# Kernel tuning notes

Hardware: AMD Instinct MI355X
Metric: run time of the kernel (lower is better)

## Reference

```python
import jax, jax.numpy as jnp
import numpy as np

NUM_BEAM, NUM_NULL, NUM_BIN, NUM_CH = 8, 4, 257, 8
NUM_BLOCK, NUM_FRAME = 8, 500
ALPHA, LOW_FREQ, HIGH_FREQ = 0.35, 5, 70


def setup_inputs() -> dict:
    key = jax.random.key(0)
    k1, k2, k3, k4 = jax.random.split(key, 4)
    return {
        "input": jax.random.normal(k1, (NUM_BLOCK, NUM_FRAME, 2, NUM_BIN, NUM_CH), jnp.float32),
        "beam_id": jax.random.randint(k2, (NUM_BLOCK,), 0, NUM_BEAM),
        "targ_w": jax.random.normal(k3, (NUM_BEAM, 2, NUM_BIN, NUM_CH), jnp.float32),
        "null_w": jax.random.normal(k4, (NUM_BEAM, NUM_NULL, 2, NUM_BIN, NUM_CH), jnp.float32),
    }


def _forward(input, beam_id, targ_w, null_w):
    a = ALPHA
    xr, xi = input[:, :, 0], input[:, :, 1]            # (B,T,F,C)
    # target beamformer: select per-block complex weights (B,2,F,C)
    tw = targ_w[beam_id]
    twr, twi = tw[:, 0], tw[:, 1]                      # (B,F,C)
    tr = jnp.einsum('btfc,bfc->btf', xr, twr) - jnp.einsum('btfc,bfc->btf', xi, twi)
    ti = jnp.einsum('btfc,bfc->btf', xr, twi) + jnp.einsum('btfc,bfc->btf', xi, twr)
    tr, ti = tr[..., None], ti[..., None]              # (B,T,F,1)
    # null beamformer: (B,N,2,F,C)
    nw = null_w[beam_id]
    nwr, nwi = nw[:, :, 0], nw[:, :, 1]                # (B,N,F,C)
    nr = jnp.einsum('btfc,bnfc->btfn', xr, nwr) - jnp.einsum('btfc,bnfc->btfn', xi, nwi)
    ni = jnp.einsum('btfc,bnfc->btfn', xr, nwi) + jnp.einsum('btfc,bnfc->btfn', xi, nwr)
    # elementwise cross-spectra products (B,T,F,N)
    pr = tr * nr + ti * ni
    pi = ti * nr - tr * ni
    pw = jnp.mean(xr ** 2 + xi ** 2, axis=-1, keepdims=True)  # (B,T,F,1)

    # t = 0 (note: (1-alpha) scales only the FIRST product, as in the source)
    phi_r0 = (1.0 - a) * tr[:, 0] * nr[:, 0] + ti[:, 0] * ni[:, 0]
    phi_i0 = (1.0 - a) * ti[:, 0] * nr[:, 0] - tr[:, 0] * ni[:, 0]
    psd0 = (1.0 - a) * pw[:, 0]
    phi0 = jnp.sqrt(phi_r0 ** 2 + phi_i0 ** 2)
    dcf0 = jnp.clip(phi0 / (psd0 + 1e-13), 0.01, 1.0)

    def step(carry, xs):
        phi_r, phi_i, psd = carry
        pr_t, pi_t, pw_t = xs
        phi_r = a * phi_r + (1.0 - a) * pr_t
        phi_i = a * phi_i + (1.0 - a) * pi_t
        psd = a * psd + (1.0 - a) * pw_t
        phi = jnp.sqrt(phi_r ** 2 + phi_i ** 2)
        dcf_t = jnp.clip(phi / (psd + 1e-13), 0.01, 1.0)
        pre = jnp.sum(psd[:, LOW_FREQ:HIGH_FREQ, :], axis=1, keepdims=True)
        aft = jnp.sum(phi[:, LOW_FREQ:HIGH_FREQ, :], axis=1, keepdims=True)
        ratio = jnp.clip(aft / (pre + 1e-10), 0.01, 1.0)
        dcf_t = jnp.sqrt(dcf_t * ratio)
        return (phi_r, phi_i, psd), dcf_t

    xs = (jnp.moveaxis(pr[:, 1:], 1, 0),
          jnp.moveaxis(pi[:, 1:], 1, 0),
          jnp.moveaxis(pw[:, 1:], 1, 0))
    _, dcf_rest = jax.lax.scan(step, (phi_r0, phi_i0, psd0), xs)  # (T-1,B,F,N)
    dcf = jnp.concatenate([dcf0[None], dcf_rest], axis=0)
    dcf = jnp.moveaxis(dcf, 0, 1)                                 # (B,T,F,N)
    targ_out = jnp.stack([tr[..., 0], ti[..., 0]], axis=2)        # (B,T,2,F)
    return dcf, targ_out


def reference(input, beam_id, targ_w, null_w):
    return _forward(input, beam_id, targ_w, null_w)
```

## Files before the change

### kernel.cpp

```cpp
#include <hip/hip_runtime.h>

#define NB 8
#define NT 500
#define NF 257
#define NC 8
#define NNUL 4
#define LOWF 5
#define HIGHF 70
#define S_CHUNK 8
#define WARM 4
#define N_CHUNK 63
#define AL 0.35f

__device__ __forceinline__ float dot8(const float4& a0, const float4& a1,
                                      const float4& b0, const float4& b1) {
    return a0.x*b0.x + a0.y*b0.y + a0.z*b0.z + a0.w*b0.w
         + a1.x*b1.x + a1.y*b1.y + a1.z*b1.z + a1.w*b1.w;
}

__global__ __launch_bounds__(1024, 4) void dcf_fused_kernel(
    const float* __restrict__ x,
    const int* __restrict__ beam_id,
    const float* __restrict__ targ_w,
    const float* __restrict__ null_w,
    float* __restrict__ out)
{
    const int tid = threadIdx.x;
    const int bid = blockIdx.x;
    const int b  = bid & 7;
    const int k  = bid >> 3;
    const int t0 = k * S_CHUNK;
    const int te = min(NT, t0 + S_CHUNK);
    int ts = t0 - WARM; if (ts < 0) ts = 0;

    const int f = tid >> 2;
    const int n = tid & 3;
    const int wid = tid >> 6;
    const int lane = tid & 63;
    const bool extra = (tid < 4);

    __shared__ float s_w256[16 + 4 * 16];
    __shared__ float s_part[S_CHUNK][25];
    __shared__ float s_dcf[S_CHUNK][1028];

    const int beam = beam_id[b];
    const int pA = n & 1;
    const int offA = pA * (NF * NC);
    const int offB = (1 - pA) * (NF * NC);
    const int psel = (n == 1 || n == 2) ? 1 : 0;
    const float nsign = pA ? -1.f : 1.f;

    float4 tw0, tw1, nwA0, nwA1, nwB0, nwB1;
    {
        const float* tp = targ_w + ((size_t)(beam * 2 + psel) * NF + f) * NC;
        tw0 = *(const float4*)(tp);  tw1 = *(const float4*)(tp + 4);
        const float* qp = null_w + ((size_t)((beam * NNUL + n) * 2) * NF + f) * NC;
        nwA0 = *(const float4*)(qp + offA);  nwA1 = *(const float4*)(qp + offA + 4);
        nwB0 = *(const float4*)(qp + offB);  nwB1 = *(const float4*)(qp + offB + 4);
    }
    if (tid < 16) {
        int p = tid >> 3, c = tid & 7;
        s_w256[tid] = targ_w[((size_t)(beam * 2 + p) * NF + 256) * NC + c];
    } else if (tid < 80) {
        int i = tid - 16;
        int nn = i >> 4, p = (i >> 3) & 1, c = i & 7;
        s_w256[tid] = null_w[((size_t)((beam * NNUL + nn) * 2 + p) * NF + 256) * NC + c];
    }
    __syncthreads();

    float phi_r = 0.f, phi_i = 0.f, psd = 0.f;
    float phi_r2 = 0.f, phi_i2 = 0.f, psd2 = 0.f;
    const float a = AL, oma = 1.0f - AL;
    const size_t rowlen = 2 * NF * NC;
    const bool in_red = (f >= LOWF) && (f < HIGHF);

    const float* xrow = x + (size_t)(b * NT + ts) * rowlen + f * NC;
    float4 pA0 = *(const float4*)(xrow + offA);
    float4 pA1 = *(const float4*)(xrow + offA + 4);
    float4 pB0 = *(const float4*)(xrow + offB);
    float4 pB1 = *(const float4*)(xrow + offB + 4);

    float* outT = out + (size_t)NB * NT * NF * NNUL;

    for (int t = ts; t < te; ++t) {
        const float4 A0 = pA0, A1 = pA1, B0 = pB0, B1 = pB1;
        if (t + 1 < te) {
            const float* xr2 = x + (size_t)(b * NT + t + 1) * rowlen + f * NC;
            pA0 = *(const float4*)(xr2 + offA);
            pA1 = *(const float4*)(xr2 + offA + 4);
            pB0 = *(const float4*)(xr2 + offB);
            pB1 = *(const float4*)(xr2 + offB + 4);
        }

        const float d = dot8(A0, A1, tw0, tw1);
        const float e = __shfl_xor(d, 1);
        const float u = (n < 2) ? ((n == 0) ? (d - e) : (e - d)) : (d + e);
        const float v = __shfl_xor(u, 2);
        const float tr = (n < 2) ? u : v;
        const float ti = (n < 2) ? v : u;

        const float P = dot8(A0, A1, nwA0, nwA1);
        const float Q = dot8(B0, B1, nwB0, nwB1);
        const float nr = nsign * (P - Q);
        const float ni = dot8(A0, A1, nwB0, nwB1) + dot8(B0, B1, nwA0, nwA1);
        const float pw = (dot8(A0, A1, A0, A1) + dot8(B0, B1, B0, B1)) * 0.125f;

        if (t == 0) {
            phi_r = oma * tr * nr + ti * ni;
            phi_i = oma * ti * nr - tr * ni;
            psd   = oma * pw;
        } else {
            phi_r = a * phi_r + oma * (tr * nr + ti * ni);
            phi_i = a * phi_i + oma * (ti * nr - tr * ni);
            psd   = a * psd + oma * pw;
        }

        float tr2 = 0.f, ti2 = 0.f;
        if (extra) {
            const float* xw = x + (size_t)(b * NT + t) * rowlen + 256 * NC;
            const float4 eA0 = *(const float4*)(xw + offA);
            const float4 eA1 = *(const float4*)(xw + offA + 4);
            const float4 eB0 = *(const float4*)(xw + offB);
            const float4 eB1 = *(const float4*)(xw + offB + 4);
            const float4 etw0 = *(const float4*)&s_w256[psel * 8];
            const float4 etw1 = *(const float4*)&s_w256[psel * 8 + 4];
            const float* nq = &s_w256[16 + n * 16];
            const float4 enA0 = *(const float4*)(nq + pA * 8);
            const float4 enA1 = *(const float4*)(nq + pA * 8 + 4);
            const float4 enB0 = *(const float4*)(nq + (1 - pA) * 8);
            const float4 enB1 = *(const float4*)(nq + (1 - pA) * 8 + 4);
            const float d2 = dot8(eA0, eA1, etw0, etw1);
            const float e2 = __shfl_xor(d2, 1);
            const float u2 = (n < 2) ? ((n == 0) ? (d2 - e2) : (e2 - d2)) : (d2 + e2);
            const float v2 = __shfl_xor(u2, 2);
            tr2 = (n < 2) ? u2 : v2;
            ti2 = (n < 2) ? v2 : u2;
            const float P2 = dot8(eA0, eA1, enA0, enA1);
            const float Q2 = dot8(eB0, eB1, enB0, enB1);
            const float nr2 = nsign * (P2 - Q2);
            const float ni2 = dot8(eA0, eA1, enB0, enB1) + dot8(eB0, eB1, enA0, enA1);
            const float pw2 = (dot8(eA0, eA1, eA0, eA1) + dot8(eB0, eB1, eB0, eB1)) * 0.125f;
            if (t == 0) {
                phi_r2 = oma * tr2 * nr2 + ti2 * ni2;
                phi_i2 = oma * ti2 * nr2 - tr2 * ni2;
                psd2   = oma * pw2;
            } else {
                phi_r2 = a * phi_r2 + oma * (tr2 * nr2 + ti2 * ni2);
                phi_i2 = a * phi_i2 + oma * (ti2 * nr2 - tr2 * ni2);
                psd2   = a * psd2 + oma * pw2;
            }
        }

        if (t >= t0) {
            const int fr = t - t0;
            const float phi = sqrtf(phi_r * phi_r + phi_i * phi_i);
            const float dcfv = fminf(fmaxf(phi / (psd + 1e-13f), 0.01f), 1.0f);
            const size_t bt = (size_t)(b * NT + t);
            if (n == 0) outT[(bt * 2 + 0) * NF + f] = tr;
            if (n == 1) outT[(bt * 2 + 1) * NF + f] = ti;
            s_dcf[fr][tid] = dcfv;
            if (extra) {
                const float phi2 = sqrtf(phi_r2 * phi_r2 + phi_i2 * phi_i2);
                const float dcf2v = fminf(fmaxf(phi2 / (psd2 + 1e-13f), 0.01f), 1.0f);
                s_dcf[fr][1024 + n] = dcf2v;
                if (n == 0) outT[(bt * 2 + 0) * NF + 256] = tr2;
                if (n == 1) outT[(bt * 2 + 1) * NF + 256] = ti2;
            }
            if (wid < 5) {
                float v_phi = in_red ? phi : 0.f;
                float v_psd = (in_red && n == 0) ? psd : 0.f;
                #pragma unroll
                for (int off = 4; off < 64; off <<= 1) {
                    v_phi += __shfl_xor(v_phi, off);
                    v_psd += __shfl_xor(v_psd, off);
                }
                if (lane < 4)  s_part[fr][wid * 5 + lane] = v_phi;
                if (lane == 0) s_part[fr][wid * 5 + 4]    = v_psd;
            }
        }
    }

    __syncthreads();

    const int nf = te - t0;
    for (int fr = 0; fr < nf; ++fr) {
        const int t = t0 + fr;
        const size_t bt = (size_t)(b * NT + t);
        float dcfv = s_dcf[fr][tid];
        float dcf2v = extra ? s_dcf[fr][1024 + n] : 0.f;
        if (t >= 1) {
            const float* sp = s_part[fr];
            const float pre = sp[4] + sp[9] + sp[14] + sp[19] + sp[24];
            const float aft = sp[n] + sp[5 + n] + sp[10 + n] + sp[15 + n] + sp[20 + n];
            const float ratio = fminf(fmaxf(aft / (pre + 1e-10f), 0.01f), 1.0f);
            dcfv = sqrtf(dcfv * ratio);
            if (extra) dcf2v = sqrtf(dcf2v * ratio);
        }
        out[(bt * NF + f) * NNUL + n] = dcfv;
        if (extra) out[(bt * NF + 256) * NNUL + n] = dcf2v;
    }
}

extern "C" void kernel_launch(void* const* d_in, const int* in_sizes, int n_in,
                              void* d_out, int out_size, void* d_ws, size_t ws_size,
                              hipStream_t stream) {
    const float* x       = (const float*)d_in[0];
    const int*   beam_id = (const int*)d_in[1];
    const float* targ_w  = (const float*)d_in[2];
    const float* null_w  = (const float*)d_in[3];
    float* out           = (float*)d_out;
    (void)d_ws; (void)ws_size;

    dcf_fused_kernel<<<dim3(NB * N_CHUNK), dim3(1024), 0, stream>>>(
        x, beam_id, targ_w, null_w, out);
}
```

Baseline: 133.9 us.

## Split each frame's channel loads across quad lanes and exchange via shuffles

Each of the four lanes in an (f, n) quad now loads a single float4 quarter of the frame's real/imag channel data instead of all four float4s. The missing pieces come from the other quad lanes through xor-1/2/3 shuffles, and the power sum is reduced across the quad. The time loop is also unrolled by two with a two-frame-deep prefetch. This cuts redundant vector memory instructions and cache traffic by roughly four times, at the cost of many extra cross-lane shuffle operations per frame.

```diff
diff --git a/kernel.cpp b/kernel.cpp
--- a/kernel.cpp
+++ b/kernel.cpp
@@ -12,10 +12,14 @@
 #define N_CHUNK 63
 #define AL 0.35f
 
-__device__ __forceinline__ float dot8(const float4& a0, const float4& a1,
-                                      const float4& b0, const float4& b1) {
-    return a0.x*b0.x + a0.y*b0.y + a0.z*b0.z + a0.w*b0.w
-         + a1.x*b1.x + a1.y*b1.y + a1.z*b1.z + a1.w*b1.w;
+__device__ __forceinline__ float dot4(const float4& a, const float4& b) {
+    return a.x*b.x + a.y*b.y + a.z*b.z + a.w*b.w;
+}
+__device__ __forceinline__ float4 shq(const float4& v, const int m) {
+    float4 r;
+    r.x = __shfl_xor(v.x, m); r.y = __shfl_xor(v.y, m);
+    r.z = __shfl_xor(v.z, m); r.w = __shfl_xor(v.w, m);
+    return r;
 }
 
 __global__ __launch_bounds__(1024, 4) void dcf_fused_kernel(
@@ -45,18 +49,22 @@
 
     const int beam = beam_id[b];
     const int pA = n & 1;
-    const int offA = pA * (NF * NC);
-    const int offB = (1 - pA) * (NF * NC);
+    const int h  = n >> 1;
+    const int co = h * 4;
+    const int cx = 4 - co;
     const int psel = (n == 1 || n == 2) ? 1 : 0;
     const float nsign = pA ? -1.f : 1.f;
-
-    float4 tw0, tw1, nwA0, nwA1, nwB0, nwB1;
+    const size_t PSTR = (size_t)NF * NC;
+
+    float4 twO, twX, nAO, nAX, nBO, nBX;
     {
         const float* tp = targ_w + ((size_t)(beam * 2 + psel) * NF + f) * NC;
-        tw0 = *(const float4*)(tp);  tw1 = *(const float4*)(tp + 4);
-        const float* qp = null_w + ((size_t)((beam * NNUL + n) * 2) * NF + f) * NC;
-        nwA0 = *(const float4*)(qp + offA);  nwA1 = *(const float4*)(qp + offA + 4);
-        nwB0 = *(const float4*)(qp + offB);  nwB1 = *(const float4*)(qp + offB + 4);
+        twO = *(const float4*)(tp + co);  twX = *(const float4*)(tp + cx);
+        const float* qp = null_w + (((size_t)(beam * NNUL + n) * 2) * NF + f) * NC;
+        nAO = *(const float4*)(qp + pA * PSTR + co);
+        nAX = *(const float4*)(qp + pA * PSTR + cx);
+        nBO = *(const float4*)(qp + (1 - pA) * PSTR + co);
+        nBX = *(const float4*)(qp + (1 - pA) * PSTR + cx);
     }
     if (tid < 16) {
         int p = tid >> 3, c = tid & 7;
@@ -71,39 +79,34 @@
     float phi_r = 0.f, phi_i = 0.f, psd = 0.f;
     float phi_r2 = 0.f, phi_i2 = 0.f, psd2 = 0.f;
     const float a = AL, oma = 1.0f - AL;
-    const size_t rowlen = 2 * NF * NC;
+    const size_t rowlen = 2 * PSTR;
     const bool in_red = (f >= LOWF) && (f < HIGHF);
 
-    const float* xrow = x + (size_t)(b * NT + ts) * rowlen + f * NC;
-    float4 pA0 = *(const float4*)(xrow + offA);
-    float4 pA1 = *(const float4*)(xrow + offA + 4);
-    float4 pB0 = *(const float4*)(xrow + offB);
-    float4 pB1 = *(const float4*)(xrow + offB + 4);
-
+    const float* xb = x + (size_t)b * NT * rowlen + pA * PSTR + (size_t)f * NC + co;
+    const float* xe = x + (size_t)b * NT * rowlen + pA * PSTR + 256 * NC + co;
     float* outT = out + (size_t)NB * NT * NF * NNUL;
 
-    for (int t = ts; t < te; ++t) {
-        const float4 A0 = pA0, A1 = pA1, B0 = pB0, B1 = pB1;
-        if (t + 1 < te) {
-            const float* xr2 = x + (size_t)(b * NT + t + 1) * rowlen + f * NC;
-            pA0 = *(const float4*)(xr2 + offA);
-            pA1 = *(const float4*)(xr2 + offA + 4);
-            pB0 = *(const float4*)(xr2 + offB);
-            pB1 = *(const float4*)(xr2 + offB + 4);
-        }
-
-        const float d = dot8(A0, A1, tw0, tw1);
+    auto frame = [&](const int t, const float4& L) {
+        const float4 X1 = shq(L, 1);
+        const float4 X2 = shq(L, 2);
+        const float4 X3 = shq(L, 3);
+
+        const float d = dot4(L, twO) + dot4(X2, twX);
         const float e = __shfl_xor(d, 1);
         const float u = (n < 2) ? ((n == 0) ? (d - e) : (e - d)) : (d + e);
         const float v = __shfl_xor(u, 2);
         const float tr = (n < 2) ? u : v;
         const float ti = (n < 2) ? v : u;
 
-        const float P = dot8(A0, A1, nwA0, nwA1);
-        const float Q = dot8(B0, B1, nwB0, nwB1);
+        const float P  = dot4(L,  nAO) + dot4(X2, nAX);
+        const float Q  = dot4(X1, nBO) + dot4(X3, nBX);
         const float nr = nsign * (P - Q);
-        const float ni = dot8(A0, A1, nwB0, nwB1) + dot8(B0, B1, nwA0, nwA1);
-        const float pw = (dot8(A0, A1, A0, A1) + dot8(B0, B1, B0, B1)) * 0.125f;
+        const float ni = dot4(L, nBO) + dot4(X2, nBX) + dot4(X1, nAO) + dot4(X3, nAX);
+
+        float s = dot4(L, L);
+        s += __shfl_xor(s, 1);
+        s += __shfl_xor(s, 2);
+        const float pw = s * 0.125f;
 
         if (t == 0) {
             phi_r = oma * tr * nr + ti * ni;
@@ -117,29 +120,31 @@
 
         float tr2 = 0.f, ti2 = 0.f;
         if (extra) {
-            const float* xw = x + (size_t)(b * NT + t) * rowlen + 256 * NC;
-            const float4 eA0 = *(const float4*)(xw + offA);
-            const float4 eA1 = *(const float4*)(xw + offA + 4);
-            const float4 eB0 = *(const float4*)(xw + offB);
-            const float4 eB1 = *(const float4*)(xw + offB + 4);
-            const float4 etw0 = *(const float4*)&s_w256[psel * 8];
-            const float4 etw1 = *(const float4*)&s_w256[psel * 8 + 4];
+            const float4 Le = *(const float4*)(xe + (size_t)t * rowlen);
+            const float4 Y1 = shq(Le, 1);
+            const float4 Y2 = shq(Le, 2);
+            const float4 Y3 = shq(Le, 3);
+            const float4 etwO = *(const float4*)&s_w256[psel * 8 + co];
+            const float4 etwX = *(const float4*)&s_w256[psel * 8 + cx];
             const float* nq = &s_w256[16 + n * 16];
-            const float4 enA0 = *(const float4*)(nq + pA * 8);
-            const float4 enA1 = *(const float4*)(nq + pA * 8 + 4);
-            const float4 enB0 = *(const float4*)(nq + (1 - pA) * 8);
-            const float4 enB1 = *(const float4*)(nq + (1 - pA) * 8 + 4);
-            const float d2 = dot8(eA0, eA1, etw0, etw1);
+            const float4 enAO = *(const float4*)(nq + pA * 8 + co);
+            const float4 enAX = *(const float4*)(nq + pA * 8 + cx);
+            const float4 enBO = *(const float4*)(nq + (1 - pA) * 8 + co);
+            const float4 enBX = *(const float4*)(nq + (1 - pA) * 8 + cx);
+            const float d2 = dot4(Le, etwO) + dot4(Y2, etwX);
             const float e2 = __shfl_xor(d2, 1);
             const float u2 = (n < 2) ? ((n == 0) ? (d2 - e2) : (e2 - d2)) : (d2 + e2);
             const float v2 = __shfl_xor(u2, 2);
             tr2 = (n < 2) ? u2 : v2;
             ti2 = (n < 2) ? v2 : u2;
-            const float P2 = dot8(eA0, eA1, enA0, enA1);
-            const float Q2 = dot8(eB0, eB1, enB0, enB1);
+            const float P2  = dot4(Le, enAO) + dot4(Y2, enAX);
+            const float Q2  = dot4(Y1, enBO) + dot4(Y3, enBX);
             const float nr2 = nsign * (P2 - Q2);
-            const float ni2 = dot8(eA0, eA1, enB0, enB1) + dot8(eB0, eB1, enA0, enA1);
-            const float pw2 = (dot8(eA0, eA1, eA0, eA1) + dot8(eB0, eB1, eB0, eB1)) * 0.125f;
+            const float ni2 = dot4(Le, enBO) + dot4(Y2, enBX) + dot4(Y1, enAO) + dot4(Y3, enAX);
+            float s2 = dot4(Le, Le);
+            s2 += __shfl_xor(s2, 1);
+            s2 += __shfl_xor(s2, 2);
+            const float pw2 = s2 * 0.125f;
             if (t == 0) {
                 phi_r2 = oma * tr2 * nr2 + ti2 * ni2;
                 phi_i2 = oma * ti2 * nr2 - tr2 * ni2;
@@ -178,6 +183,15 @@
                 if (lane == 0) s_part[fr][wid * 5 + 4]    = v_psd;
             }
         }
+    };
+
+    float4 La = *(const float4*)(xb + (size_t)ts * rowlen);
+    float4 Lb = *(const float4*)(xb + (size_t)(ts + 1) * rowlen);
+    for (int t = ts; t < te; t += 2) {
+        frame(t, La);
+        if (t + 2 < te) La = *(const float4*)(xb + (size_t)(t + 2) * rowlen);
+        frame(t + 1, Lb);
+        if (t + 3 < te) Lb = *(const float4*)(xb + (size_t)(t + 3) * rowlen);
     }
 
     __syncthreads();
```

Measured after the change: 138.9 us. 1.04x slower.
